# Kernel tuning notes

Measured on AMD Instinct MI355X. Metric: run time of the kernel, lower is better.

The kernel has to match this reference:

```python
import jax, jax.numpy as jnp
import numpy as np

B, S, E, D, H, DH, FF, NL = 16384, 4, 1152, 192, 4, 48, 768, 2


def _ln(x, w, b, eps=1e-5):
    m = jnp.mean(x, axis=-1, keepdims=True)
    v = jnp.mean((x - m) ** 2, axis=-1, keepdims=True)
    return (x - m) * jax.lax.rsqrt(v + eps) * w + b


def _gelu(x):
    # torch nn.GELU / TransformerEncoderLayer(activation='gelu') use exact erf GELU
    return jax.nn.gelu(x, approximate=False)


def _pos_enc():
    pos = np.arange(S, dtype=np.float32)[:, None]
    div = np.exp(np.arange(0, D, 2, dtype=np.float32) * (-np.log(10000.0) / D))
    pe = np.zeros((S, D), dtype=np.float32)
    pe[:, 0::2] = np.sin(pos * div)
    pe[:, 1::2] = np.cos(pos * div)
    return jnp.asarray(pe)


def setup_inputs() -> dict:
    key = jax.random.key(0)
    ks = jax.random.split(key, 16)
    w = lambda k, shape: jax.random.normal(k, shape, jnp.float32) * 0.05
    return {
        'embeddings': jax.random.normal(ks[0], (B, S, E), jnp.float32),
        'in_ln_w': jnp.ones((E,), jnp.float32), 'in_ln_b': jnp.zeros((E,), jnp.float32),
        'in_proj_w': w(ks[1], (D, E)), 'in_proj_b': jnp.zeros((D,), jnp.float32),
        'qkv_w': w(ks[2], (NL, 3 * D, D)), 'qkv_b': jnp.zeros((NL, 3 * D), jnp.float32),
        'attn_out_w': w(ks[3], (NL, D, D)), 'attn_out_b': jnp.zeros((NL, D), jnp.float32),
        'ln1_w': jnp.ones((NL, D), jnp.float32), 'ln1_b': jnp.zeros((NL, D), jnp.float32),
        'ln2_w': jnp.ones((NL, D), jnp.float32), 'ln2_b': jnp.zeros((NL, D), jnp.float32),
        'ff1_w': w(ks[4], (NL, FF, D)), 'ff1_b': jnp.zeros((NL, FF), jnp.float32),
        'ff2_w': w(ks[5], (NL, D, FF)), 'ff2_b': jnp.zeros((NL, D), jnp.float32),
        'head_ln_w': jnp.ones((D,), jnp.float32), 'head_ln_b': jnp.zeros((D,), jnp.float32),
        'h1_w': w(ks[6], (256, D)), 'h1_b': jnp.zeros((256,), jnp.float32),
        'h2_w': w(ks[7], (64, 256)), 'h2_b': jnp.zeros((64,), jnp.float32),
        'h3_w': w(ks[8], (1, 64)) * 0.1, 'h3_b': jnp.zeros((1,), jnp.float32),
    }


def reference(embeddings, in_ln_w, in_ln_b, in_proj_w, in_proj_b,
              qkv_w, qkv_b, attn_out_w, attn_out_b,
              ln1_w, ln1_b, ln2_w, ln2_b,
              ff1_w, ff1_b, ff2_w, ff2_b,
              head_ln_w, head_ln_b, h1_w, h1_b, h2_w, h2_b, h3_w, h3_b):
    # input_proj: LN -> Linear(E, D) -> GELU (dropout is identity in eval)
    x = _ln(embeddings, in_ln_w, in_ln_b)
    x = _gelu(x @ in_proj_w.T + in_proj_b)
    # sinusoidal positional encoding
    x = x + _pos_enc()[None]
    scale = 1.0 / jnp.sqrt(jnp.float32(DH))
    # norm_first TransformerEncoder layers
    for i in range(NL):
        xn = _ln(x, ln1_w[i], ln1_b[i])
        qkv = xn @ qkv_w[i].T + qkv_b[i]                       # (B, S, 3D)
        q, k, v = jnp.split(qkv, 3, axis=-1)
        q = q.reshape(B, S, H, DH)
        k = k.reshape(B, S, H, DH)
        v = v.reshape(B, S, H, DH)
        scores = jnp.einsum('bqhd,bkhd->bhqk', q, k) * scale   # (B, H, S, S)
        attn = jax.nn.softmax(scores, axis=-1)
        o = jnp.einsum('bhqk,bkhd->bqhd', attn, v).reshape(B, S, D)
        x = x + (o @ attn_out_w[i].T + attn_out_b[i])
        xn = _ln(x, ln2_w[i], ln2_b[i])
        x = x + (_gelu(xn @ ff1_w[i].T + ff1_b[i]) @ ff2_w[i].T + ff2_b[i])
    pooled = x.mean(axis=1)                                    # (B, D)
    h = _ln(pooled, head_ln_w, head_ln_b)
    h = _gelu(h @ h1_w.T + h1_b)
    h = _gelu(h @ h2_w.T + h2_b)
    return (h @ h3_w.T + h3_b)[:, 0]                           # (B,)
```

## Files before the change

kernel.cpp:

```cpp
#include <hip/hip_runtime.h>
#include <hip/hip_bf16.h>
#include <math.h>

#define B_   16384
#define S_   4
#define E_   1152
#define D_   192
#define FF_  768
#define NL_  2
#define MTOK (B_ * S_)

typedef __attribute__((ext_vector_type(8))) _Float16 half8;
typedef __attribute__((ext_vector_type(4))) float floatx4;

__device__ __forceinline__ float gelu_f(float x) {
  return 0.5f * x * (1.0f + erff(x * 0.70710678118654752f));
}

__global__ __launch_bounds__(256) void cvt_f16_kernel(const float* __restrict__ s,
                                                      _Float16* __restrict__ d) {
  int i = (blockIdx.x * 256 + threadIdx.x) * 8;
  float4 a = *(const float4*)(s + i);
  float4 b = *(const float4*)(s + i + 4);
  half8 h;
// ... 11 lines not shown
  const float* Wr = W + (size_t)n * 1152;
  _Float16* Whr = Wh + (size_t)n * 1152;
  float s1 = 0.f, s2 = 0.f;
  #pragma unroll
  for (int j = 0; j < 18; ++j) {
    int k = lane + 64 * j;
    float wv = Wr[k];
    _Float16 h = (_Float16)(wv * g[k]);
    Whr[k] = h;
    s1 += (float)h;
    s2 = fmaf(b[k], wv, s2);
  }
  #pragma unroll
  for (int off = 1; off < 64; off <<= 1) {
    s1 += __shfl_xor(s1, off);
    s2 += __shfl_xor(s2, off);
  }
  if (lane == 0) { c1[n] = s1; c2[n] = s2 + bias[n]; }
}

__global__ __launch_bounds__(256) void inproj2_kernel(
    const float* __restrict__ emb, const _Float16* __restrict__ whp,
    const float* __restrict__ c1g, const float* __restrict__ c2g,
    float* __restrict__ xout, float* __restrict__ stD) {
  __shared__ __align__(16) _Float16 As[64][72];
  __shared__ float stats_[64][2];
  __shared__ float red_[4][64][2];
  __shared__ float pe_[4][192];
  const int tid = threadIdx.x;
  const int m0 = blockIdx.x * 64;
  const int w = tid >> 6, lane = tid & 63;
  const int ln16 = lane & 15, quad = lane >> 4;
  const int r_a = tid >> 2;
  const int c_a = (tid & 3) * 16;

  for (int i = tid; i < 768; i += 256) {
    int r = i / 192, col = i - r * 192;
    float ang = (float)r * expf((float)(col & ~1) * (-0.047970522770709292f));
    pe_[r][col] = (col & 1) ? cosf(ang) : sinf(ang);
  }

  const float* Arow = emb + (size_t)(m0 + r_a) * 1152 + c_a;
  const _Float16* wb = whp + (size_t)(w * 48 + ln16) * 1152 + quad * 8;

  float4 pa[4];
  auto loadA = [&](int k0) {
    #pragma unroll
    for (int j = 0; j < 4; ++j) pa[j] = *(const float4*)(Arow + k0 + j * 4);
  };

// ... 41 lines not shown

  s += __shfl_xor(s, 1); s += __shfl_xor(s, 2);
  q += __shfl_xor(q, 1); q += __shfl_xor(q, 2);
  if ((tid & 3) == 0) {
    float mean = s * (1.f / 1152.f);
    stats_[r_a][0] = mean;
    stats_[r_a][1] = rsqrtf(q * (1.f / 1152.f) - mean * mean + 1e-5f);
  }
  __syncthreads();

  float c1v[3], c2v[3];
  #pragma unroll
  for (int nt = 0; nt < 3; ++nt) {
    c1v[nt] = c1g[w * 48 + nt * 16 + ln16];
    c2v[nt] = c2g[w * 48 + nt * 16 + ln16];
  }
  float* xg = xout + (size_t)m0 * 192;
  #pragma unroll
  for (int mt = 0; mt < 4; ++mt) {
    #pragma unroll
    for (int r = 0; r < 4; ++r) {
      const int row = mt * 16 + quad * 4 + r;
      const float rm = stats_[row][0], rr = stats_[row][1];
      float so = 0.f, qo = 0.f;
      #pragma unroll
      for (int nt = 0; nt < 3; ++nt) {
        const int col = w * 48 + nt * 16 + ln16;
        float v = rr * (acc[mt][nt][r] - rm * c1v[nt]) + c2v[nt];
        v = gelu_f(v);
        v += pe_[r][col];
        xg[(size_t)row * 192 + col] = v;
        so += v;
        qo = fmaf(v, v, qo);
      }
      so += __shfl_xor(so, 1); so += __shfl_xor(so, 2);
      so += __shfl_xor(so, 4); so += __shfl_xor(so, 8);
      qo += __shfl_xor(qo, 1); qo += __shfl_xor(qo, 2);
      qo += __shfl_xor(qo, 4); qo += __shfl_xor(qo, 8);
      if (ln16 == 0) { red_[w][row][0] = so; red_[w][row][1] = qo; }
    }
  }
  __syncthreads();
  if (tid < 64) {
    float so = red_[0][tid][0] + red_[1][tid][0] + red_[2][tid][0] + red_[3][tid][0];
    float qo = red_[0][tid][1] + red_[1][tid][1] + red_[2][tid][1] + red_[3][tid][1];
    float mean = so * (1.f / 192.f);
    stD[2 * (m0 + tid)] = mean;
    stD[2 * (m0 + tid) + 1] = rsqrtf(qo * (1.f / 192.f) - mean * mean + 1e-5f);
  }
}

__global__ __launch_bounds__(256) void layer_attn_kernel(
    float* __restrict__ x, const _Float16* __restrict__ wqkv,
    const float* __restrict__ bqkv, const _Float16* __restrict__ wao,
    const float* __restrict__ bao, const float* __restrict__ ln1g,
    const float* __restrict__ ln1b_, float* __restrict__ stD) {
  __shared__ __align__(16) _Float16 xh[32][200];
  __shared__ __align__(16) _Float16 qk[32][584];
  __shared__ float sp[8][4][4][4];
  const int tid = threadIdx.x;
  const int m0 = blockIdx.x * 32;
  const int w = tid >> 6, lane = tid & 63;
  const int ln16 = lane & 15, quad = lane >> 4;

  {
    const int ra = tid >> 3, ca = (tid & 7) * 24;
    const float sm = stD[2 * (m0 + ra)], srs = stD[2 * (m0 + ra) + 1];
    const float* Ar = x + (size_t)(m0 + ra) * 192 + ca;
    #pragma unroll
    for (int j = 0; j < 3; ++j) {
      float4 a0 = *(const float4*)(Ar + j * 8);
      float4 a1 = *(const float4*)(Ar + j * 8 + 4);
      float4 g0 = *(const float4*)(ln1g + ca + j * 8);
      float4 g1 = *(const float4*)(ln1g + ca + j * 8 + 4);
      float4 b0 = *(const float4*)(ln1b_ + ca + j * 8);
      float4 b1 = *(const float4*)(ln1b_ + ca + j * 8 + 4);
      half8 h;
      h[0] = (_Float16)((a0.x - sm) * srs * g0.x + b0.x);
      h[1] = (_Float16)((a0.y - sm) * srs * g0.y + b0.y);
      h[2] = (_Float16)((a0.z - sm) * srs * g0.z + b0.z);
      h[3] = (_Float16)((a0.w - sm) * srs * g0.w + b0.w);
      h[4] = (_Float16)((a1.x - sm) * srs * g1.x + b1.x);
      h[5] = (_Float16)((a1.y - sm) * srs * g1.y + b1.y);
      h[6] = (_Float16)((a1.z - sm) * srs * g1.z + b1.z);
      h[7] = (_Float16)((a1.w - sm) * srs * g1.w + b1.w);
      *(half8*)&xh[ra][ca + j * 8] = h;
    }
  }
  __syncthreads();

  for (int nt = 0; nt < 9; ++nt) {
    const int nc = w * 144 + nt * 16;
    half8 bf[6];
    const _Float16* wp = wqkv + (size_t)(nc + ln16) * 192 + quad * 8;
    #pragma unroll
    for (int k = 0; k < 6; ++k) bf[k] = *(const half8*)(wp + k * 32);
    floatx4 a0v = {}, a1v = {};
    #pragma unroll
    for (int k = 0; k < 6; ++k) {
      half8 f0 = *(const half8*)&xh[ln16][k * 32 + quad * 8];
      half8 f1 = *(const half8*)&xh[16 + ln16][k * 32 + quad * 8];
      a0v = __builtin_amdgcn_mfma_f32_16x16x32_f16(f0, bf[k], a0v, 0, 0, 0);
      a1v = __builtin_amdgcn_mfma_f32_16x16x32_f16(f1, bf[k], a1v, 0, 0, 0);
    }
    const float bv = bqkv[nc + ln16];
    #pragma unroll
    for (int r = 0; r < 4; ++r) {
      qk[quad * 4 + r][nc + ln16]      = (_Float16)(a0v[r] + bv);
      qk[16 + quad * 4 + r][nc + ln16] = (_Float16)(a1v[r] + bv);
    }
  }
  __syncthreads();

  #pragma unroll
  for (int s2 = 0; s2 < 2; ++s2) {
    const int sg = w * 2 + s2;
    const int h = lane >> 4, i = (lane >> 2) & 3, j = lane & 3;
    const _Float16* qp = &qk[4 * sg + i][h * 48];
    const _Float16* kp = &qk[4 * sg + j][192 + h * 48];
    float s = 0.f;
    #pragma unroll
    for (int d = 0; d < 6; ++d) {
      half8 qv = *(const half8*)(qp + d * 8);
      half8 kv = *(const half8*)(kp + d * 8);
      #pragma unroll
      for (int e = 0; e < 8; ++e) s += (float)qv[e] * (float)kv[e];
    }
    s *= 0.14433756729740643f;
    float mx = fmaxf(s, __shfl_xor(s, 1));
    mx = fmaxf(mx, __shfl_xor(mx, 2));
    float e = expf(s - mx);
    float sum = e + __shfl_xor(e, 1);
    sum += __shfl_xor(sum, 2);
    sp[sg][h][i][j] = e / sum;
  }
  #pragma unroll
  for (int s2 = 0; s2 < 2; ++s2) {
    const int sg = w * 2 + s2;
    #pragma unroll
    for (int ii = 0; ii < 4; ++ii) {
      #pragma unroll
      for (int cc = 0; cc < 3; ++cc) {
        const int c = lane + cc * 64;
        const int hh = c / 48;
        float a = 0.f;
        #pragma unroll
        for (int jj = 0; jj < 4; ++jj)
          a += sp[sg][hh][ii][jj] * (float)qk[4 * sg + jj][384 + c];
        xh[4 * sg + ii][c] = (_Float16)a;
      }
    }
  }
  __syncthreads();

  float* outs = (float*)&qk[0][0];
  #pragma unroll
  for (int nt = 0; nt < 3; ++nt) {
    const int nc = w * 48 + nt * 16;
    half8 bf[6];
    const _Float16* wp = wao + (size_t)(nc + ln16) * 192 + quad * 8;
    #pragma unroll
    for (int k = 0; k < 6; ++k) bf[k] = *(const half8*)(wp + k * 32);
    floatx4 a0v = {}, a1v = {};
    #pragma unroll
    for (int k = 0; k < 6; ++k) {
      half8 f0 = *(const half8*)&xh[ln16][k * 32 + quad * 8];
      half8 f1 = *(const half8*)&xh[16 + ln16][k * 32 + quad * 8];
      a0v = __builtin_amdgcn_mfma_f32_16x16x32_f16(f0, bf[k], a0v, 0, 0, 0);
      a1v = __builtin_amdgcn_mfma_f32_16x16x32_f16(f1, bf[k], a1v, 0, 0, 0);
    }
    const float bv = bao[nc + ln16];
    #pragma unroll
    for (int r = 0; r < 4; ++r) {
      outs[(quad * 4 + r) * 192 + nc + ln16]      = a0v[r] + bv;
      outs[(16 + quad * 4 + r) * 192 + nc + ln16] = a1v[r] + bv;
    }
  }
  __syncthreads();

  {
    const int fbase = tid * 6;
    const int row = tid >> 3;
    float* xg = x + (size_t)m0 * 192;
    float s = 0.f, q = 0.f;
    #pragma unroll
    for (int j = 0; j < 6; ++j) {
      float4 v = ((const float4*)outs)[fbase + j];
      float4 rr = *(const float4*)(xg + (fbase + j) * 4);
      v.x += rr.x; v.y += rr.y; v.z += rr.z; v.w += rr.w;
      s += v.x + v.y + v.z + v.w;
      q += v.x * v.x + v.y * v.y + v.z * v.z + v.w * v.w;
      *(float4*)(xg + (fbase + j) * 4) = v;
    }
    s += __shfl_xor(s, 1); s += __shfl_xor(s, 2); s += __shfl_xor(s, 4);
    q += __shfl_xor(q, 1); q += __shfl_xor(q, 2); q += __shfl_xor(q, 4);
    if ((tid & 7) == 0) {
      float mean = s * (1.f / 192.f);
      stD[2 * (m0 + row)] = mean;
      stD[2 * (m0 + row) + 1] = rsqrtf(q * (1.f / 192.f) - mean * mean + 1e-5f);
    }
  }
}

__global__ __launch_bounds__(256) void layer_ff_kernel(
    float* __restrict__ x, const _Float16* __restrict__ wff1,
    const float* __restrict__ bff1, const _Float16* __restrict__ wff2,
    const float* __restrict__ bff2, const float* __restrict__ ln2g,
    const float* __restrict__ ln2b_, float* __restrict__ stD) {
  __shared__ __align__(16) _Float16 xh2[64][200];
  __shared__ __align__(16) _Float16 ffh[64][392];
  const int tid = threadIdx.x;
  const int m0 = blockIdx.x * 64;
  const int w = tid >> 6, lane = tid & 63;
  const int ln16 = lane & 15, quad = lane >> 4;

  {
    const int ra = tid >> 2, ca = (tid & 3) * 48;
    const float sm = stD[2 * (m0 + ra)], srs = stD[2 * (m0 + ra) + 1];
    const float* Ar = x + (size_t)(m0 + ra) * 192 + ca;
    #pragma unroll
    for (int j = 0; j < 6; ++j) {
      float4 a0 = *(const float4*)(Ar + j * 8);
      float4 a1 = *(const float4*)(Ar + j * 8 + 4);
      float4 g0 = *(const float4*)(ln2g + ca + j * 8);
      float4 g1 = *(const float4*)(ln2g + ca + j * 8 + 4);
      float4 b0 = *(const float4*)(ln2b_ + ca + j * 8);
      float4 b1 = *(const float4*)(ln2b_ + ca + j * 8 + 4);
      half8 h;
      h[0] = (_Float16)((a0.x - sm) * srs * g0.x + b0.x);
      h[1] = (_Float16)((a0.y - sm) * srs * g0.y + b0.y);
      h[2] = (_Float16)((a0.z - sm) * srs * g0.z + b0.z);
      h[3] = (_Float16)((a0.w - sm) * srs * g0.w + b0.w);
      h[4] = (_Float16)((a1.x - sm) * srs * g1.x + b1.x);
      h[5] = (_Float16)((a1.y - sm) * srs * g1.y + b1.y);
      h[6] = (_Float16)((a1.z - sm) * srs * g1.z + b1.z);
      h[7] = (_Float16)((a1.w - sm) * srs * g1.w + b1.w);
      *(half8*)&xh2[ra][ca + j * 8] = h;
    }
  }
  __syncthreads();

  floatx4 acc2[4][3] = {};
  for (int half = 0; half < 2; ++half) {
    #pragma unroll
    for (int nt = 0; nt < 6; ++nt) {
      const int ng = half * 384 + w * 96 + nt * 16;
      const int nl = w * 96 + nt * 16;
      half8 bf[6];
      const _Float16* wp = wff1 + (size_t)(ng + ln16) * 192 + quad * 8;
      #pragma unroll
      for (int k = 0; k < 6; ++k) bf[k] = *(const half8*)(wp + k * 32);
      floatx4 a4[4] = {};
      #pragma unroll
      for (int k = 0; k < 6; ++k) {
        #pragma unroll
        for (int mt = 0; mt < 4; ++mt) {
          half8 af = *(const half8*)&xh2[mt * 16 + ln16][k * 32 + quad * 8];
          a4[mt] = __builtin_amdgcn_mfma_f32_16x16x32_f16(af, bf[k], a4[mt], 0, 0, 0);
        }
      }
      const float bv = bff1[ng + ln16];
      #pragma unroll
      for (int mt = 0; mt < 4; ++mt)
        #pragma unroll
        for (int r = 0; r < 4; ++r)
          ffh[mt * 16 + quad * 4 + r][nl + ln16] = (_Float16)gelu_f(a4[mt][r] + bv);
    }
    __syncthreads();
    for (int k12 = 0; k12 < 12; ++k12) {
      half8 af[4];
      #pragma unroll
      for (int mt = 0; mt < 4; ++mt)
        af[mt] = *(const half8*)&ffh[mt * 16 + ln16][k12 * 32 + quad * 8];
      #pragma unroll
      for (int nt = 0; nt < 3; ++nt) {
        const int nc = w * 48 + nt * 16;
        half8 bf = *(const half8*)(wff2 + (size_t)(nc + ln16) * 768 +
                                   half * 384 + k12 * 32 + quad * 8);
        #pragma unroll
        for (int mt = 0; mt < 4; ++mt)
          acc2[mt][nt] = __builtin_amdgcn_mfma_f32_16x16x32_f16(
              af[mt], bf, acc2[mt][nt], 0, 0, 0);
      }
    }
    __syncthreads();
  }

  float* outs = (float*)&ffh[0][0];
  #pragma unroll
  for (int nt = 0; nt < 3; ++nt) {
    const int nc = w * 48 + nt * 16;
    const float bv = bff2[nc + ln16];
    #pragma unroll
    for (int mt = 0; mt < 4; ++mt)
      #pragma unroll
      for (int r = 0; r < 4; ++r)
        outs[(mt * 16 + quad * 4 + r) * 192 + nc + ln16] = acc2[mt][nt][r] + bv;
  }
  __syncthreads();

  {
    const int fbase = tid * 12;
    const int row = tid >> 2;
    float* xg = x + (size_t)m0 * 192;
    float s = 0.f, q = 0.f;
    #pragma unroll
    for (int j = 0; j < 12; ++j) {
      float4 v = ((const float4*)outs)[fbase + j];
      float4 rr = *(const float4*)(xg + (fbase + j) * 4);
      v.x += rr.x; v.y += rr.y; v.z += rr.z; v.w += rr.w;
      s += v.x + v.y + v.z + v.w;
      q += v.x * v.x + v.y * v.y + v.z * v.z + v.w * v.w;
      *(float4*)(xg + (fbase + j) * 4) = v;
    }
    s += __shfl_xor(s, 1); s += __shfl_xor(s, 2);
    q += __shfl_xor(q, 1); q += __shfl_xor(q, 2);
    if ((tid & 3) == 0) {
      float mean = s * (1.f / 192.f);
      stD[2 * (m0 + row)] = mean;
      stD[2 * (m0 + row) + 1] = rsqrtf(q * (1.f / 192.f) - mean * mean + 1e-5f);
    }
  }
}

template <int EPI>
__global__ __launch_bounds__(256) void gemm_f32(
    const float* __restrict__ A, const float* __restrict__ W,
    const float* __restrict__ bias, float* __restrict__ C,
    int M, int N, int K) {
  __shared__ float As[16][68];
  __shared__ float Bs[16][68];
  const int tid = threadIdx.x;
  const int m0 = blockIdx.x * 64;
  const int n0 = blockIdx.y * 64;
  const int tx = tid & 15, ty = tid >> 4;
  const int lr = tid >> 2;
  const int lk = (tid & 3) << 2;
  float acc[4][4] = {};
  const float* Arow = A + (size_t)(m0 + lr) * K;
  const float* Wrow = W + (size_t)(n0 + lr) * K;
  for (int k0 = 0; k0 < K; k0 += 16) {
    float4 av = *(const float4*)(Arow + k0 + lk);
    float4 wv = *(const float4*)(Wrow + k0 + lk);
    __syncthreads();
    As[lk + 0][lr] = av.x; As[lk + 1][lr] = av.y;
    As[lk + 2][lr] = av.z; As[lk + 3][lr] = av.w;
    Bs[lk + 0][lr] = wv.x; Bs[lk + 1][lr] = wv.y;
    Bs[lk + 2][lr] = wv.z; Bs[lk + 3][lr] = wv.w;
    __syncthreads();
    #pragma unroll
    for (int kk = 0; kk < 16; ++kk) {
      float4 a = *(const float4*)&As[kk][ty * 4];
      float4 b = *(const float4*)&Bs[kk][tx * 4];
      acc[0][0] += a.x * b.x; acc[0][1] += a.x * b.y; acc[0][2] += a.x * b.z; acc[0][3] += a.x * b.w;
      acc[1][0] += a.y * b.x; acc[1][1] += a.y * b.y; acc[1][2] += a.y * b.z; acc[1][3] += a.y * b.w;
      acc[2][0] += a.z * b.x; acc[2][1] += a.z * b.y; acc[2][2] += a.z * b.z; acc[2][3] += a.z * b.w;
      acc[3][0] += a.w * b.x; acc[3][1] += a.w * b.y; acc[3][2] += a.w * b.z; acc[3][3] += a.w * b.w;
    }
  }
  float4 bv = *(const float4*)(bias + n0 + tx * 4);
  #pragma unroll
  for (int i = 0; i < 4; ++i) {
    int m = m0 + ty * 4 + i;
    float v0 = acc[i][0] + bv.x, v1 = acc[i][1] + bv.y;
    float v2 = acc[i][2] + bv.z, v3 = acc[i][3] + bv.w;
    if constexpr (EPI == 1) {
      v0 = gelu_f(v0); v1 = gelu_f(v1); v2 = gelu_f(v2); v3 = gelu_f(v3);
    }
    float4 ov; ov.x = v0; ov.y = v1; ov.z = v2; ov.w = v3;
    *(float4*)(C + (size_t)m * N + n0 + tx * 4) = ov;
  }
}

__global__ __launch_bounds__(256) void pool_ln_kernel(const float* __restrict__ x,
                                                      const float* __restrict__ g,
                                                      const float* __restrict__ b,
                                                      float* __restrict__ hout) {
  int bi = blockIdx.x * 4 + (threadIdx.x >> 6);
  int lane = threadIdx.x & 63;
  const float* row = x + (size_t)bi * 4 * D_;
  float vals[3];
  float sum = 0.f;
  #pragma unroll
  for (int cc = 0; cc < 3; ++cc) {
    int d = lane + cc * 64;
    float v = 0.25f * (row[d] + row[D_ + d] + row[2 * D_ + d] + row[3 * D_ + d]);
    vals[cc] = v; sum += v;
  }
  #pragma unroll
  for (int off = 1; off < 64; off <<= 1) sum += __shfl_xor(sum, off);
  float mean = sum / (float)D_;
  float vs = 0.f;
  #pragma unroll
  for (int cc = 0; cc < 3; ++cc) { float d0 = vals[cc] - mean; vs += d0 * d0; }
  #pragma unroll
  for (int off = 1; off < 64; off <<= 1) vs += __shfl_xor(vs, off);
  float rstd = rsqrtf(vs / (float)D_ + 1e-5f);
  #pragma unroll
  for (int cc = 0; cc < 3; ++cc) {
    int d = lane + cc * 64;
    hout[(size_t)bi * D_ + d] = (vals[cc] - mean) * rstd * g[d] + b[d];
  }
}

__global__ __launch_bounds__(256) void head_final_kernel(const float* __restrict__ h2,
                                                         const float* __restrict__ w,
                                                         const float* __restrict__ b,
                                                         float* __restrict__ out) {
  int bi = blockIdx.x * 4 + (threadIdx.x >> 6);
  int lane = threadIdx.x & 63;
  float v = h2[(size_t)bi * 64 + lane] * w[lane];
  #pragma unroll
  for (int off = 1; off < 64; off <<= 1) v += __shfl_xor(v, off);
  if (lane == 0) out[bi] = v + b[0];
}

extern "C" void kernel_launch(void* const* d_in, const int* in_sizes, int n_in,
                              void* d_out, int out_size, void* d_ws, size_t ws_size,
                              hipStream_t stream) {
  (void)in_sizes; (void)n_in; (void)out_size; (void)ws_size;
  const float* emb       = (const float*)d_in[0];
  const float* in_ln_w   = (const float*)d_in[1];
  const float* in_ln_b   = (const float*)d_in[2];
  const float* in_proj_w = (const float*)d_in[3];
  const float* in_proj_b = (const float*)d_in[4];
  const float* qkv_w     = (const float*)d_in[5];
  const float* qkv_b     = (const float*)d_in[6];
  const float* aow       = (const float*)d_in[7];
  const float* aob       = (const float*)d_in[8];
  const float* ln1w      = (const float*)d_in[9];
  const float* ln1b      = (const float*)d_in[10];
  const float* ln2w      = (const float*)d_in[11];
  const float* ln2b      = (const float*)d_in[12];
  const float* ff1w      = (const float*)d_in[13];
  const float* ff1b      = (const float*)d_in[14];
  const float* ff2w      = (const float*)d_in[15];
  const float* ff2b      = (const float*)d_in[16];
  const float* hlnw      = (const float*)d_in[17];
  const float* hlnb      = (const float*)d_in[18];
  const float* h1w       = (const float*)d_in[19];
  const float* h1b       = (const float*)d_in[20];
  const float* h2w       = (const float*)d_in[21];
  const float* h2b       = (const float*)d_in[22];
  const float* h3w       = (const float*)d_in[23];
  const float* h3b       = (const float*)d_in[24];
  float* out = (float*)d_out;

  float* ws = (float*)d_ws;
  size_t off = 0;
  float* x   = ws + off; off += (size_t)MTOK * D_;
  float* stD = ws + off; off += (size_t)MTOK * 2;
  float* hp  = ws + off; off += (size_t)B_ * D_;
  float* h1  = ws + off; off += (size_t)B_ * 256;
  float* h2  = ws + off; off += (size_t)B_ * 64;
  float* c1  = ws + off; off += 192;
  float* c2  = ws + off; off += 192;
  _Float16* wh = (_Float16*)(ws + off);
  _Float16* w_inproj = wh;
  _Float16* w_qkv    = w_inproj + 221184;
  _Float16* w_ao     = w_qkv    + 221184;
  _Float16* w_ff1    = w_ao     + 73728;
  _Float16* w_ff2    = w_ff1    + 294912;

  prep_inproj_w<<<48, 256, 0, stream>>>(in_proj_w, in_ln_w, in_ln_b, in_proj_b,
                                        w_inproj, c1, c2);
  cvt_f16_kernel<<<221184 / 2048, 256, 0, stream>>>(qkv_w, w_qkv);
  cvt_f16_kernel<<<73728  / 2048, 256, 0, stream>>>(aow, w_ao);
  cvt_f16_kernel<<<294912 / 2048, 256, 0, stream>>>(ff1w, w_ff1);
  cvt_f16_kernel<<<294912 / 2048, 256, 0, stream>>>(ff2w, w_ff2);

  inproj2_kernel<<<MTOK / 64, 256, 0, stream>>>(emb, w_inproj, c1, c2, x, stD);

  for (int i = 0; i < NL_; ++i) {
    layer_attn_kernel<<<MTOK / 32, 256, 0, stream>>>(
        x, w_qkv + (size_t)i * 110592, qkv_b + (size_t)i * 576,
        w_ao + (size_t)i * 36864, aob + (size_t)i * 192,
        ln1w + (size_t)i * 192, ln1b + (size_t)i * 192, stD);
    layer_ff_kernel<<<MTOK / 64, 256, 0, stream>>>(
        x, w_ff1 + (size_t)i * 147456, ff1b + (size_t)i * 768,
        w_ff2 + (size_t)i * 147456, ff2b + (size_t)i * 192,
        ln2w + (size_t)i * 192, ln2b + (size_t)i * 192, stD);
  }

  pool_ln_kernel<<<B_ / 4, 256, 0, stream>>>(x, hlnw, hlnb, hp);
  gemm_f32<1><<<dim3(B_ / 64, 256 / 64), 256, 0, stream>>>(hp, h1w, h1b, h1, B_, 256, D_);
  gemm_f32<1><<<dim3(B_ / 64, 64 / 64), 256, 0, stream>>>(h1, h2w, h2b, h2, B_, 64, 256);
  head_final_kernel<<<B_ / 4, 256, 0, stream>>>(h2, h3w, h3b, out);
}
```

Before: 996.4 us.

## Fuse both encoder layers, pooling and regression head into one register-resident kernel

Replaces the per-layer attention and feed-forward kernels, pooling, two fp32 head GEMMs and the final reduction with a single kernel. Each 32-token block keeps its residual stream in registers across both layers and computes LayerNorm statistics in place, so x and the stats buffer are no longer written and re-read through global memory. The head MLP now runs in fp16 MFMA with pre-converted weights. In exchange, the FF stage uses 32-row tiles (less weight reuse per block than the previous 64-row tiles), register pressure goes up, and the head carries fp16 rounding and zero-padded MFMA rows.

```diff
diff --git a/kernel.cpp b/kernel.cpp
--- a/kernel.cpp
+++ b/kernel.cpp
@@ -57,10 +57,9 @@
 __global__ __launch_bounds__(256) void inproj2_kernel(
     const float* __restrict__ emb, const _Float16* __restrict__ whp,
     const float* __restrict__ c1g, const float* __restrict__ c2g,
-    float* __restrict__ xout, float* __restrict__ stD) {
+    float* __restrict__ xout) {
   __shared__ __align__(16) _Float16 As[64][72];
   __shared__ float stats_[64][2];
-  __shared__ float red_[4][64][2];
   __shared__ float pe_[4][192];
   const int tid = threadIdx.x;
   const int m0 = blockIdx.x * 64;
@@ -148,7 +147,6 @@
     for (int r = 0; r < 4; ++r) {
       const int row = mt * 16 + quad * 4 + r;
       const float rm = stats_[row][0], rr = stats_[row][1];
-      float so = 0.f, qo = 0.f;
       #pragma unroll
       for (int nt = 0; nt < 3; ++nt) {
         const int col = w * 48 + nt * 16 + ln16;
@@ -156,31 +154,24 @@
         v = gelu_f(v);
         v += pe_[r][col];
         xg[(size_t)row * 192 + col] = v;
-        so += v;
-        qo = fmaf(v, v, qo);
-      }
-      so += __shfl_xor(so, 1); so += __shfl_xor(so, 2);
-      so += __shfl_xor(so, 4); so += __shfl_xor(so, 8);
-      qo += __shfl_xor(qo, 1); qo += __shfl_xor(qo, 2);
-      qo += __shfl_xor(qo, 4); qo += __shfl_xor(qo, 8);
-      if (ln16 == 0) { red_[w][row][0] = so; red_[w][row][1] = qo; }
-    }
-  }
-  __syncthreads();
-  if (tid < 64) {
-    float so = red_[0][tid][0] + red_[1][tid][0] + red_[2][tid][0] + red_[3][tid][0];
-    float qo = red_[0][tid][1] + red_[1][tid][1] + red_[2][tid][1] + red_[3][tid][1];
-    float mean = so * (1.f / 192.f);
-    stD[2 * (m0 + tid)] = mean;
-    stD[2 * (m0 + tid) + 1] = rsqrtf(qo * (1.f / 192.f) - mean * mean + 1e-5f);
+      }
+    }
   }
 }
 
-__global__ __launch_bounds__(256) void layer_attn_kernel(
-    float* __restrict__ x, const _Float16* __restrict__ wqkv,
-    const float* __restrict__ bqkv, const _Float16* __restrict__ wao,
-    const float* __restrict__ bao, const float* __restrict__ ln1g,
-    const float* __restrict__ ln1b_, float* __restrict__ stD) {
+__global__ __launch_bounds__(256) void mega_kernel(
+    const float* __restrict__ x,
+    const _Float16* __restrict__ wqkv0, const float* __restrict__ bqkv0,
+    const _Float16* __restrict__ wao0,  const float* __restrict__ bao0,
+    const _Float16* __restrict__ wff10, const float* __restrict__ bff10,
+    const _Float16* __restrict__ wff20, const float* __restrict__ bff20,
+    const float* __restrict__ ln1g0, const float* __restrict__ ln1b0,
+    const float* __restrict__ ln2g0, const float* __restrict__ ln2b0,
+    const float* __restrict__ hlng, const float* __restrict__ hlnb,
+    const _Float16* __restrict__ h1wh, const float* __restrict__ h1b,
+    const _Float16* __restrict__ h2wh, const float* __restrict__ h2b,
+    const float* __restrict__ h3w, const float* __restrict__ h3b,
+    float* __restrict__ out) {
   __shared__ __align__(16) _Float16 xh[32][200];
   __shared__ __align__(16) _Float16 qk[32][584];
   __shared__ float sp[8][4][4][4];
@@ -188,357 +179,315 @@
   const int m0 = blockIdx.x * 32;
   const int w = tid >> 6, lane = tid & 63;
   const int ln16 = lane & 15, quad = lane >> 4;
-
+  const int row = tid >> 3, cg = tid & 7;
+  const int ca = cg * 24;
+
+  float4 xr[6];
   {
-    const int ra = tid >> 3, ca = (tid & 7) * 24;
-    const float sm = stD[2 * (m0 + ra)], srs = stD[2 * (m0 + ra) + 1];
-    const float* Ar = x + (size_t)(m0 + ra) * 192 + ca;
-    #pragma unroll
-    for (int j = 0; j < 3; ++j) {
-      float4 a0 = *(const float4*)(Ar + j * 8);
-      float4 a1 = *(const float4*)(Ar + j * 8 + 4);
-      float4 g0 = *(const float4*)(ln1g + ca + j * 8);
-      float4 g1 = *(const float4*)(ln1g + ca + j * 8 + 4);
-      float4 b0 = *(const float4*)(ln1b_ + ca + j * 8);
-      float4 b1 = *(const float4*)(ln1b_ + ca + j * 8 + 4);
-      half8 h;
-      h[0] = (_Float16)((a0.x - sm) * srs * g0.x + b0.x);
-      h[1] = (_Float16)((a0.y - sm) * srs * g0.y + b0.y);
-      h[2] = (_Float16)((a0.z - sm) * srs * g0.z + b0.z);
-      h[3] = (_Float16)((a0.w - sm) * srs * g0.w + b0.w);
-      h[4] = (_Float16)((a1.x - sm) * srs * g1.x + b1.x);
-      h[5] = (_Float16)((a1.y - sm) * srs * g1.y + b1.y);
-      h[6] = (_Float16)((a1.z - sm) * srs * g1.z + b1.z);
-      h[7] = (_Float16)((a1.w - sm) * srs * g1.w + b1.w);
-      *(half8*)&xh[ra][ca + j * 8] = h;
-    }
-  }
-  __syncthreads();
-
-  for (int nt = 0; nt < 9; ++nt) {
-    const int nc = w * 144 + nt * 16;
-    half8 bf[6];
-    const _Float16* wp = wqkv + (size_t)(nc + ln16) * 192 + quad * 8;
-    #pragma unroll
-    for (int k = 0; k < 6; ++k) bf[k] = *(const half8*)(wp + k * 32);
-    floatx4 a0v = {}, a1v = {};
-    #pragma unroll
-    for (int k = 0; k < 6; ++k) {
-      half8 f0 = *(const half8*)&xh[ln16][k * 32 + quad * 8];
-      half8 f1 = *(const half8*)&xh[16 + ln16][k * 32 + quad * 8];
-      a0v = __builtin_amdgcn_mfma_f32_16x16x32_f16(f0, bf[k], a0v, 0, 0, 0);
-      a1v = __builtin_amdgcn_mfma_f32_16x16x32_f16(f1, bf[k], a1v, 0, 0, 0);
-    }
-    const float bv = bqkv[nc + ln16];
-    #pragma unroll
-    for (int r = 0; r < 4; ++r) {
-      qk[quad * 4 + r][nc + ln16]      = (_Float16)(a0v[r] + bv);
-      qk[16 + quad * 4 + r][nc + ln16] = (_Float16)(a1v[r] + bv);
-    }
-  }
-  __syncthreads();
-
-  #pragma unroll
-  for (int s2 = 0; s2 < 2; ++s2) {
-    const int sg = w * 2 + s2;
-    const int h = lane >> 4, i = (lane >> 2) & 3, j = lane & 3;
-    const _Float16* qp = &qk[4 * sg + i][h * 48];
-    const _Float16* kp = &qk[4 * sg + j][192 + h * 48];
-    float s = 0.f;
-    #pragma unroll
-    for (int d = 0; d < 6; ++d) {
-      half8 qv = *(const half8*)(qp + d * 8);
-      half8 kv = *(const half8*)(kp + d * 8);
-      #pragma unroll
-      for (int e = 0; e < 8; ++e) s += (float)qv[e] * (float)kv[e];
-    }
-    s *= 0.14433756729740643f;
-    float mx = fmaxf(s, __shfl_xor(s, 1));
-    mx = fmaxf(mx, __shfl_xor(mx, 2));
-    float e = expf(s - mx);
-    float sum = e + __shfl_xor(e, 1);
-    sum += __shfl_xor(sum, 2);
-    sp[sg][h][i][j] = e / sum;
-  }
-  #pragma unroll
-  for (int s2 = 0; s2 < 2; ++s2) {
-    const int sg = w * 2 + s2;
-    #pragma unroll
-    for (int ii = 0; ii < 4; ++ii) {
-      #pragma unroll
-      for (int cc = 0; cc < 3; ++cc) {
-        const int c = lane + cc * 64;
-        const int hh = c / 48;
-        float a = 0.f;
-        #pragma unroll
-        for (int jj = 0; jj < 4; ++jj)
-          a += sp[sg][hh][ii][jj] * (float)qk[4 * sg + jj][384 + c];
-        xh[4 * sg + ii][c] = (_Float16)a;
-      }
-    }
-  }
-  __syncthreads();
-
-  float* outs = (float*)&qk[0][0];
-  #pragma unroll
-  for (int nt = 0; nt < 3; ++nt) {
-    const int nc = w * 48 + nt * 16;
-    half8 bf[6];
-    const _Float16* wp = wao + (size_t)(nc + ln16) * 192 + quad * 8;
-    #pragma unroll
-    for (int k = 0; k < 6; ++k) bf[k] = *(const half8*)(wp + k * 32);
-    floatx4 a0v = {}, a1v = {};
-    #pragma unroll
-    for (int k = 0; k < 6; ++k) {
-      half8 f0 = *(const half8*)&xh[ln16][k * 32 + quad * 8];
-      half8 f1 = *(const half8*)&xh[16 + ln16][k * 32 + quad * 8];
-      a0v = __builtin_amdgcn_mfma_f32_16x16x32_f16(f0, bf[k], a0v, 0, 0, 0);
-      a1v = __builtin_amdgcn_mfma_f32_16x16x32_f16(f1, bf[k], a1v, 0, 0, 0);
-    }
-    const float bv = bao[nc + ln16];
-    #pragma unroll
-    for (int r = 0; r < 4; ++r) {
-      outs[(quad * 4 + r) * 192 + nc + ln16]      = a0v[r] + bv;
-      outs[(16 + quad * 4 + r) * 192 + nc + ln16] = a1v[r] + bv;
-    }
-  }
-  __syncthreads();
-
-  {
-    const int fbase = tid * 6;
-    const int row = tid >> 3;
-    float* xg = x + (size_t)m0 * 192;
+    const float* Ar = x + (size_t)(m0 + row) * 192 + ca;
+    #pragma unroll
+    for (int j = 0; j < 6; ++j) xr[j] = *(const float4*)(Ar + j * 4);
+  }
+
+  auto ln_to_xh = [&](const float* g, const float* bb) {
     float s = 0.f, q = 0.f;
     #pragma unroll
     for (int j = 0; j < 6; ++j) {
-      float4 v = ((const float4*)outs)[fbase + j];
-      float4 rr = *(const float4*)(xg + (fbase + j) * 4);
-      v.x += rr.x; v.y += rr.y; v.z += rr.z; v.w += rr.w;
+      float4 v = xr[j];
       s += v.x + v.y + v.z + v.w;
-      q += v.x * v.x + v.y * v.y + v.z * v.z + v.w * v.w;
-      *(float4*)(xg + (fbase + j) * 4) = v;
+      q = fmaf(v.x, v.x, q); q = fmaf(v.y, v.y, q);
+      q = fmaf(v.z, v.z, q); q = fmaf(v.w, v.w, q);
     }
     s += __shfl_xor(s, 1); s += __shfl_xor(s, 2); s += __shfl_xor(s, 4);
     q += __shfl_xor(q, 1); q += __shfl_xor(q, 2); q += __shfl_xor(q, 4);
-    if ((tid & 7) == 0) {
-      float mean = s * (1.f / 192.f);
-      stD[2 * (m0 + row)] = mean;
-      stD[2 * (m0 + row) + 1] = rsqrtf(q * (1.f / 192.f) - mean * mean + 1e-5f);
-    }
-  }
-}
-
-__global__ __launch_bounds__(256) void layer_ff_kernel(
-    float* __restrict__ x, const _Float16* __restrict__ wff1,
-    const float* __restrict__ bff1, const _Float16* __restrict__ wff2,
-    const float* __restrict__ bff2, const float* __restrict__ ln2g,
-    const float* __restrict__ ln2b_, float* __restrict__ stD) {
-  __shared__ __align__(16) _Float16 xh2[64][200];
-  __shared__ __align__(16) _Float16 ffh[64][392];
-  const int tid = threadIdx.x;
-  const int m0 = blockIdx.x * 64;
-  const int w = tid >> 6, lane = tid & 63;
-  const int ln16 = lane & 15, quad = lane >> 4;
-
-  {
-    const int ra = tid >> 2, ca = (tid & 3) * 48;
-    const float sm = stD[2 * (m0 + ra)], srs = stD[2 * (m0 + ra) + 1];
-    const float* Ar = x + (size_t)(m0 + ra) * 192 + ca;
-    #pragma unroll
-    for (int j = 0; j < 6; ++j) {
-      float4 a0 = *(const float4*)(Ar + j * 8);
-      float4 a1 = *(const float4*)(Ar + j * 8 + 4);
-      float4 g0 = *(const float4*)(ln2g + ca + j * 8);
-      float4 g1 = *(const float4*)(ln2g + ca + j * 8 + 4);
-      float4 b0 = *(const float4*)(ln2b_ + ca + j * 8);
-      float4 b1 = *(const float4*)(ln2b_ + ca + j * 8 + 4);
+    const float mean = s * (1.f / 192.f);
+    const float rs = rsqrtf(q * (1.f / 192.f) - mean * mean + 1e-5f);
+    #pragma unroll
+    for (int j = 0; j < 3; ++j) {
+      float4 a0 = xr[2 * j], a1 = xr[2 * j + 1];
+      float4 g0 = *(const float4*)(g + ca + j * 8);
+      float4 g1 = *(const float4*)(g + ca + j * 8 + 4);
+      float4 b0 = *(const float4*)(bb + ca + j * 8);
+      float4 b1 = *(const float4*)(bb + ca + j * 8 + 4);
       half8 h;
-      h[0] = (_Float16)((a0.x - sm) * srs * g0.x + b0.x);
-      h[1] = (_Float16)((a0.y - sm) * srs * g0.y + b0.y);
-      h[2] = (_Float16)((a0.z - sm) * srs * g0.z + b0.z);
-      h[3] = (_Float16)((a0.w - sm) * srs * g0.w + b0.w);
-      h[4] = (_Float16)((a1.x - sm) * srs * g1.x + b1.x);
-      h[5] = (_Float16)((a1.y - sm) * srs * g1.y + b1.y);
-      h[6] = (_Float16)((a1.z - sm) * srs * g1.z + b1.z);
-      h[7] = (_Float16)((a1.w - sm) * srs * g1.w + b1.w);
-      *(half8*)&xh2[ra][ca + j * 8] = h;
-    }
-  }
-  __syncthreads();
-
-  floatx4 acc2[4][3] = {};
-  for (int half = 0; half < 2; ++half) {
-    #pragma unroll
-    for (int nt = 0; nt < 6; ++nt) {
-      const int ng = half * 384 + w * 96 + nt * 16;
-      const int nl = w * 96 + nt * 16;
+      h[0] = (_Float16)((a0.x - mean) * rs * g0.x + b0.x);
+      h[1] = (_Float16)((a0.y - mean) * rs * g0.y + b0.y);
+      h[2] = (_Float16)((a0.z - mean) * rs * g0.z + b0.z);
+      h[3] = (_Float16)((a0.w - mean) * rs * g0.w + b0.w);
+      h[4] = (_Float16)((a1.x - mean) * rs * g1.x + b1.x);
+      h[5] = (_Float16)((a1.y - mean) * rs * g1.y + b1.y);
+      h[6] = (_Float16)((a1.z - mean) * rs * g1.z + b1.z);
+      h[7] = (_Float16)((a1.w - mean) * rs * g1.w + b1.w);
+      *(half8*)&xh[row][ca + j * 8] = h;
+    }
+  };
+
+  for (int l = 0; l < NL_; ++l) {
+    const _Float16* wqkv = wqkv0 + (size_t)l * 110592;
+    const float*    bqkv = bqkv0 + (size_t)l * 576;
+    const _Float16* wao  = wao0  + (size_t)l * 36864;
+    const float*    bao  = bao0  + (size_t)l * 192;
+    const _Float16* wff1 = wff10 + (size_t)l * 147456;
+    const float*    bff1 = bff10 + (size_t)l * 768;
+    const _Float16* wff2 = wff20 + (size_t)l * 147456;
+    const float*    bff2 = bff20 + (size_t)l * 192;
+
+    ln_to_xh(ln1g0 + l * 192, ln1b0 + l * 192);
+    __syncthreads();
+
+    for (int nt = 0; nt < 9; ++nt) {
+      const int nc = w * 144 + nt * 16;
       half8 bf[6];
-      const _Float16* wp = wff1 + (size_t)(ng + ln16) * 192 + quad * 8;
+      const _Float16* wp = wqkv + (size_t)(nc + ln16) * 192 + quad * 8;
       #pragma unroll
       for (int k = 0; k < 6; ++k) bf[k] = *(const half8*)(wp + k * 32);
-      floatx4 a4[4] = {};
+      floatx4 a0v = {}, a1v = {};
       #pragma unroll
       for (int k = 0; k < 6; ++k) {
-        #pragma unroll
-        for (int mt = 0; mt < 4; ++mt) {
-          half8 af = *(const half8*)&xh2[mt * 16 + ln16][k * 32 + quad * 8];
-          a4[mt] = __builtin_amdgcn_mfma_f32_16x16x32_f16(af, bf[k], a4[mt], 0, 0, 0);
+        half8 f0 = *(const half8*)&xh[ln16][k * 32 + quad * 8];
+        half8 f1 = *(const half8*)&xh[16 + ln16][k * 32 + quad * 8];
+        a0v = __builtin_amdgcn_mfma_f32_16x16x32_f16(f0, bf[k], a0v, 0, 0, 0);
+        a1v = __builtin_amdgcn_mfma_f32_16x16x32_f16(f1, bf[k], a1v, 0, 0, 0);
+      }
+      const float bv = bqkv[nc + ln16];
+      #pragma unroll
+      for (int r = 0; r < 4; ++r) {
+        qk[quad * 4 + r][nc + ln16]      = (_Float16)(a0v[r] + bv);
+        qk[16 + quad * 4 + r][nc + ln16] = (_Float16)(a1v[r] + bv);
+      }
+    }
+    __syncthreads();
+
+    #pragma unroll
+    for (int s2 = 0; s2 < 2; ++s2) {
+      const int sg = w * 2 + s2;
+      const int hh = lane >> 4, i = (lane >> 2) & 3, j = lane & 3;
+      const _Float16* qp = &qk[4 * sg + i][hh * 48];
+      const _Float16* kp = &qk[4 * sg + j][192 + hh * 48];
+      float s = 0.f;
+      #pragma unroll
+      for (int d = 0; d < 6; ++d) {
+        half8 qv = *(const half8*)(qp + d * 8);
+        half8 kv = *(const half8*)(kp + d * 8);
+        #pragma unroll
+        for (int e = 0; e < 8; ++e) s += (float)qv[e] * (float)kv[e];
+      }
+      s *= 0.14433756729740643f;
+      float mx = fmaxf(s, __shfl_xor(s, 1));
+      mx = fmaxf(mx, __shfl_xor(mx, 2));
+      float e = expf(s - mx);
+      float sum = e + __shfl_xor(e, 1);
+      sum += __shfl_xor(sum, 2);
+      sp[sg][hh][i][j] = e / sum;
+    }
+    #pragma unroll
+    for (int s2 = 0; s2 < 2; ++s2) {
+      const int sg = w * 2 + s2;
+      #pragma unroll
+      for (int ii = 0; ii < 4; ++ii) {
+        #pragma unroll
+        for (int cc = 0; cc < 3; ++cc) {
+          const int c = lane + cc * 64;
+          const int hh = c / 48;
+          float a = 0.f;
+          #pragma unroll
+          for (int jj = 0; jj < 4; ++jj)
+            a += sp[sg][hh][ii][jj] * (float)qk[4 * sg + jj][384 + c];
+          xh[4 * sg + ii][c] = (_Float16)a;
         }
       }
-      const float bv = bff1[ng + ln16];
-      #pragma unroll
-      for (int mt = 0; mt < 4; ++mt)
-        #pragma unroll
-        for (int r = 0; r < 4; ++r)
-          ffh[mt * 16 + quad * 4 + r][nl + ln16] = (_Float16)gelu_f(a4[mt][r] + bv);
-    }
-    __syncthreads();
-    for (int k12 = 0; k12 < 12; ++k12) {
-      half8 af[4];
-      #pragma unroll
-      for (int mt = 0; mt < 4; ++mt)
-        af[mt] = *(const half8*)&ffh[mt * 16 + ln16][k12 * 32 + quad * 8];
+    }
+    __syncthreads();
+
+    float* outs = (float*)&qk[0][0];
+    #pragma unroll
+    for (int nt = 0; nt < 3; ++nt) {
+      const int nc = w * 48 + nt * 16;
+      half8 bf[6];
+      const _Float16* wp = wao + (size_t)(nc + ln16) * 192 + quad * 8;
+      #pragma unroll
+      for (int k = 0; k < 6; ++k) bf[k] = *(const half8*)(wp + k * 32);
+      floatx4 a0v = {}, a1v = {};
+      #pragma unroll
+      for (int k = 0; k < 6; ++k) {
+        half8 f0 = *(const half8*)&xh[ln16][k * 32 + quad * 8];
+        half8 f1 = *(const half8*)&xh[16 + ln16][k * 32 + quad * 8];
+        a0v = __builtin_amdgcn_mfma_f32_16x16x32_f16(f0, bf[k], a0v, 0, 0, 0);
+        a1v = __builtin_amdgcn_mfma_f32_16x16x32_f16(f1, bf[k], a1v, 0, 0, 0);
+      }
+      const float bv = bao[nc + ln16];
+      #pragma unroll
+      for (int r = 0; r < 4; ++r) {
+        outs[(quad * 4 + r) * 192 + nc + ln16]      = a0v[r] + bv;
+        outs[(16 + quad * 4 + r) * 192 + nc + ln16] = a1v[r] + bv;
+      }
+    }
+    __syncthreads();
+
+    {
+      const float* os = (const float*)&qk[0][0] + row * 192 + ca;
+      #pragma unroll
+      for (int j = 0; j < 6; ++j) {
+        float4 o4 = *(const float4*)(os + j * 4);
+        xr[j].x += o4.x; xr[j].y += o4.y; xr[j].z += o4.z; xr[j].w += o4.w;
+      }
+    }
+    ln_to_xh(ln2g0 + l * 192, ln2b0 + l * 192);
+    __syncthreads();
+
+    floatx4 acc2[2][3] = {};
+    _Float16 (*ffh)[392] = (_Float16 (*)[392])&qk[0][0];
+    for (int hf = 0; hf < 2; ++hf) {
+      #pragma unroll
+      for (int nt = 0; nt < 6; ++nt) {
+        const int ng = hf * 384 + w * 96 + nt * 16;
+        const int nl = w * 96 + nt * 16;
+        half8 bf[6];
+        const _Float16* wp = wff1 + (size_t)(ng + ln16) * 192 + quad * 8;
+        #pragma unroll
+        for (int k = 0; k < 6; ++k) bf[k] = *(const half8*)(wp + k * 32);
+        floatx4 a4[2] = {};
+        #pragma unroll
+        for (int k = 0; k < 6; ++k) {
+          #pragma unroll
+          for (int mt = 0; mt < 2; ++mt) {
+            half8 af = *(const half8*)&xh[mt * 16 + ln16][k * 32 + quad * 8];
+            a4[mt] = __builtin_amdgcn_mfma_f32_16x16x32_f16(af, bf[k], a4[mt], 0, 0, 0);
+          }
+        }
+        const float bv = bff1[ng + ln16];
+        #pragma unroll
+        for (int mt = 0; mt < 2; ++mt)
+          #pragma unroll
+          for (int r = 0; r < 4; ++r)
+            ffh[mt * 16 + quad * 4 + r][nl + ln16] = (_Float16)gelu_f(a4[mt][r] + bv);
+      }
+      __syncthreads();
+      for (int k12 = 0; k12 < 12; ++k12) {
+        half8 af[2];
+        #pragma unroll
+        for (int mt = 0; mt < 2; ++mt)
+          af[mt] = *(const half8*)&ffh[mt * 16 + ln16][k12 * 32 + quad * 8];
+        #pragma unroll
+        for (int nt = 0; nt < 3; ++nt) {
+          const int nc = w * 48 + nt * 16;
+          half8 bf = *(const half8*)(wff2 + (size_t)(nc + ln16) * 768 +
+                                     hf * 384 + k12 * 32 + quad * 8);
+          #pragma unroll
+          for (int mt = 0; mt < 2; ++mt)
+            acc2[mt][nt] = __builtin_amdgcn_mfma_f32_16x16x32_f16(
+                af[mt], bf, acc2[mt][nt], 0, 0, 0);
+        }
+      }
+      __syncthreads();
+    }
+    {
+      float* outs2 = (float*)&qk[0][0];
       #pragma unroll
       for (int nt = 0; nt < 3; ++nt) {
         const int nc = w * 48 + nt * 16;
-        half8 bf = *(const half8*)(wff2 + (size_t)(nc + ln16) * 768 +
-                                   half * 384 + k12 * 32 + quad * 8);
-        #pragma unroll
-        for (int mt = 0; mt < 4; ++mt)
-          acc2[mt][nt] = __builtin_amdgcn_mfma_f32_16x16x32_f16(
-              af[mt], bf, acc2[mt][nt], 0, 0, 0);
-      }
-    }
-    __syncthreads();
-  }
-
-  float* outs = (float*)&ffh[0][0];
+        const float bv = bff2[nc + ln16];
+        #pragma unroll
+        for (int mt = 0; mt < 2; ++mt)
+          #pragma unroll
+          for (int r = 0; r < 4; ++r)
+            outs2[(mt * 16 + quad * 4 + r) * 192 + nc + ln16] = acc2[mt][nt][r] + bv;
+      }
+    }
+    __syncthreads();
+    {
+      const float* os = (const float*)&qk[0][0] + row * 192 + ca;
+      #pragma unroll
+      for (int j = 0; j < 6; ++j) {
+        float4 o4 = *(const float4*)(os + j * 4);
+        xr[j].x += o4.x; xr[j].y += o4.y; xr[j].z += o4.z; xr[j].w += o4.w;
+      }
+    }
+    __syncthreads();
+  }
+
+  {
+    float* xs = (float*)&qk[0][0];
+    #pragma unroll
+    for (int j = 0; j < 6; ++j)
+      *(float4*)(xs + row * 192 + ca + j * 4) = xr[j];
+  }
+  __syncthreads();
+  _Float16 (*ph)[200] = (_Float16 (*)[200])&xh[0][0];
+  {
+    const float* xs = (const float*)&qk[0][0];
+    const int s = tid >> 5, u = tid & 31;
+    float pv[6];
+    float ss = 0.f, qq = 0.f;
+    #pragma unroll
+    for (int c6 = 0; c6 < 6; ++c6) {
+      const int c = u * 6 + c6;
+      float v = 0.25f * (xs[(4 * s) * 192 + c] + xs[(4 * s + 1) * 192 + c] +
+                         xs[(4 * s + 2) * 192 + c] + xs[(4 * s + 3) * 192 + c]);
+      pv[c6] = v; ss += v; qq = fmaf(v, v, qq);
+    }
+    ss += __shfl_xor(ss, 1); ss += __shfl_xor(ss, 2); ss += __shfl_xor(ss, 4);
+    ss += __shfl_xor(ss, 8); ss += __shfl_xor(ss, 16);
+    qq += __shfl_xor(qq, 1); qq += __shfl_xor(qq, 2); qq += __shfl_xor(qq, 4);
+    qq += __shfl_xor(qq, 8); qq += __shfl_xor(qq, 16);
+    const float mean = ss * (1.f / 192.f);
+    const float rs = rsqrtf(qq * (1.f / 192.f) - mean * mean + 1e-5f);
+    #pragma unroll
+    for (int c6 = 0; c6 < 6; ++c6) {
+      const int c = u * 6 + c6;
+      ph[s][c] = (_Float16)((pv[c6] - mean) * rs * hlng[c] + hlnb[c]);
+      ph[8 + s][c] = (_Float16)0.f;
+    }
+  }
+  __syncthreads();
+  _Float16 (*h1s)[264] = (_Float16 (*)[264])&qk[0][0];
   #pragma unroll
-  for (int nt = 0; nt < 3; ++nt) {
-    const int nc = w * 48 + nt * 16;
-    const float bv = bff2[nc + ln16];
-    #pragma unroll
-    for (int mt = 0; mt < 4; ++mt)
-      #pragma unroll
-      for (int r = 0; r < 4; ++r)
-        outs[(mt * 16 + quad * 4 + r) * 192 + nc + ln16] = acc2[mt][nt][r] + bv;
+  for (int nt = 0; nt < 4; ++nt) {
+    const int nc = w * 64 + nt * 16;
+    half8 bf[6];
+    const _Float16* wp = h1wh + (size_t)(nc + ln16) * 192 + quad * 8;
+    #pragma unroll
+    for (int k = 0; k < 6; ++k) bf[k] = *(const half8*)(wp + k * 32);
+    floatx4 a4 = {};
+    #pragma unroll
+    for (int k = 0; k < 6; ++k) {
+      half8 af = *(const half8*)&ph[ln16][k * 32 + quad * 8];
+      a4 = __builtin_amdgcn_mfma_f32_16x16x32_f16(af, bf[k], a4, 0, 0, 0);
+    }
+    const float bv = h1b[nc + ln16];
+    #pragma unroll
+    for (int r = 0; r < 4; ++r) {
+      const int rr = quad * 4 + r;
+      h1s[rr][nc + ln16] = (rr < 8) ? (_Float16)gelu_f(a4[r] + bv) : (_Float16)0.f;
+    }
   }
   __syncthreads();
-
+  _Float16 (*h2s)[72] = (_Float16 (*)[72])((char*)&qk[0][0] + 16384);
   {
-    const int fbase = tid * 12;
-    const int row = tid >> 2;
-    float* xg = x + (size_t)m0 * 192;
-    float s = 0.f, q = 0.f;
-    #pragma unroll
-    for (int j = 0; j < 12; ++j) {
-      float4 v = ((const float4*)outs)[fbase + j];
-      float4 rr = *(const float4*)(xg + (fbase + j) * 4);
-      v.x += rr.x; v.y += rr.y; v.z += rr.z; v.w += rr.w;
-      s += v.x + v.y + v.z + v.w;
-      q += v.x * v.x + v.y * v.y + v.z * v.z + v.w * v.w;
-      *(float4*)(xg + (fbase + j) * 4) = v;
-    }
-    s += __shfl_xor(s, 1); s += __shfl_xor(s, 2);
-    q += __shfl_xor(q, 1); q += __shfl_xor(q, 2);
-    if ((tid & 3) == 0) {
-      float mean = s * (1.f / 192.f);
-      stD[2 * (m0 + row)] = mean;
-      stD[2 * (m0 + row) + 1] = rsqrtf(q * (1.f / 192.f) - mean * mean + 1e-5f);
-    }
-  }
-}
-
-template <int EPI>
-__global__ __launch_bounds__(256) void gemm_f32(
-    const float* __restrict__ A, const float* __restrict__ W,
-    const float* __restrict__ bias, float* __restrict__ C,
-    int M, int N, int K) {
-  __shared__ float As[16][68];
-  __shared__ float Bs[16][68];
-  const int tid = threadIdx.x;
-  const int m0 = blockIdx.x * 64;
-  const int n0 = blockIdx.y * 64;
-  const int tx = tid & 15, ty = tid >> 4;
-  const int lr = tid >> 2;
-  const int lk = (tid & 3) << 2;
-  float acc[4][4] = {};
-  const float* Arow = A + (size_t)(m0 + lr) * K;
-  const float* Wrow = W + (size_t)(n0 + lr) * K;
-  for (int k0 = 0; k0 < K; k0 += 16) {
-    float4 av = *(const float4*)(Arow + k0 + lk);
-    float4 wv = *(const float4*)(Wrow + k0 + lk);
-    __syncthreads();
-    As[lk + 0][lr] = av.x; As[lk + 1][lr] = av.y;
-    As[lk + 2][lr] = av.z; As[lk + 3][lr] = av.w;
-    Bs[lk + 0][lr] = wv.x; Bs[lk + 1][lr] = wv.y;
-    Bs[lk + 2][lr] = wv.z; Bs[lk + 3][lr] = wv.w;
-    __syncthreads();
-    #pragma unroll
-    for (int kk = 0; kk < 16; ++kk) {
-      float4 a = *(const float4*)&As[kk][ty * 4];
-      float4 b = *(const float4*)&Bs[kk][tx * 4];
-      acc[0][0] += a.x * b.x; acc[0][1] += a.x * b.y; acc[0][2] += a.x * b.z; acc[0][3] += a.x * b.w;
-      acc[1][0] += a.y * b.x; acc[1][1] += a.y * b.y; acc[1][2] += a.y * b.z; acc[1][3] += a.y * b.w;
-      acc[2][0] += a.z * b.x; acc[2][1] += a.z * b.y; acc[2][2] += a.z * b.z; acc[2][3] += a.z * b.w;
-      acc[3][0] += a.w * b.x; acc[3][1] += a.w * b.y; acc[3][2] += a.w * b.z; acc[3][3] += a.w * b.w;
-    }
-  }
-  float4 bv = *(const float4*)(bias + n0 + tx * 4);
-  #pragma unroll
-  for (int i = 0; i < 4; ++i) {
-    int m = m0 + ty * 4 + i;
-    float v0 = acc[i][0] + bv.x, v1 = acc[i][1] + bv.y;
-    float v2 = acc[i][2] + bv.z, v3 = acc[i][3] + bv.w;
-    if constexpr (EPI == 1) {
-      v0 = gelu_f(v0); v1 = gelu_f(v1); v2 = gelu_f(v2); v3 = gelu_f(v3);
-    }
-    float4 ov; ov.x = v0; ov.y = v1; ov.z = v2; ov.w = v3;
-    *(float4*)(C + (size_t)m * N + n0 + tx * 4) = ov;
-  }
-}
-
-__global__ __launch_bounds__(256) void pool_ln_kernel(const float* __restrict__ x,
-                                                      const float* __restrict__ g,
-                                                      const float* __restrict__ b,
-                                                      float* __restrict__ hout) {
-  int bi = blockIdx.x * 4 + (threadIdx.x >> 6);
-  int lane = threadIdx.x & 63;
-  const float* row = x + (size_t)bi * 4 * D_;
-  float vals[3];
-  float sum = 0.f;
-  #pragma unroll
-  for (int cc = 0; cc < 3; ++cc) {
-    int d = lane + cc * 64;
-    float v = 0.25f * (row[d] + row[D_ + d] + row[2 * D_ + d] + row[3 * D_ + d]);
-    vals[cc] = v; sum += v;
-  }
-  #pragma unroll
-  for (int off = 1; off < 64; off <<= 1) sum += __shfl_xor(sum, off);
-  float mean = sum / (float)D_;
-  float vs = 0.f;
-  #pragma unroll
-  for (int cc = 0; cc < 3; ++cc) { float d0 = vals[cc] - mean; vs += d0 * d0; }
-  #pragma unroll
-  for (int off = 1; off < 64; off <<= 1) vs += __shfl_xor(vs, off);
-  float rstd = rsqrtf(vs / (float)D_ + 1e-5f);
-  #pragma unroll
-  for (int cc = 0; cc < 3; ++cc) {
-    int d = lane + cc * 64;
-    hout[(size_t)bi * D_ + d] = (vals[cc] - mean) * rstd * g[d] + b[d];
-  }
-}
-
-__global__ __launch_bounds__(256) void head_final_kernel(const float* __restrict__ h2,
-                                                         const float* __restrict__ w,
-                                                         const float* __restrict__ b,
-                                                         float* __restrict__ out) {
-  int bi = blockIdx.x * 4 + (threadIdx.x >> 6);
-  int lane = threadIdx.x & 63;
-  float v = h2[(size_t)bi * 64 + lane] * w[lane];
-  #pragma unroll
-  for (int off = 1; off < 64; off <<= 1) v += __shfl_xor(v, off);
-  if (lane == 0) out[bi] = v + b[0];
+    const int nc = w * 16;
+    floatx4 a4 = {};
+    #pragma unroll
+    for (int k = 0; k < 8; ++k) {
+      half8 af = *(const half8*)&h1s[ln16][k * 32 + quad * 8];
+      half8 bf = *(const half8*)(h2wh + (size_t)(nc + ln16) * 256 + k * 32 + quad * 8);
+      a4 = __builtin_amdgcn_mfma_f32_16x16x32_f16(af, bf, a4, 0, 0, 0);
+    }
+    const float bv = h2b[nc + ln16];
+    #pragma unroll
+    for (int r = 0; r < 4; ++r) {
+      const int rr = quad * 4 + r;
+      if (rr < 8) h2s[rr][nc + ln16] = (_Float16)gelu_f(a4[r] + bv);
+    }
+  }
+  __syncthreads();
+  {
+    const int s = tid >> 5, u = tid & 31;
+    float v = (float)h2s[s][2 * u] * h3w[2 * u] +
+              (float)h2s[s][2 * u + 1] * h3w[2 * u + 1];
+    v += __shfl_xor(v, 1); v += __shfl_xor(v, 2); v += __shfl_xor(v, 4);
+    v += __shfl_xor(v, 8); v += __shfl_xor(v, 16);
+    if (u == 0) out[blockIdx.x * 8 + s] = v + h3b[0];
+  }
 }
 
 extern "C" void kernel_launch(void* const* d_in, const int* in_sizes, int n_in,
@@ -575,10 +524,6 @@
   float* ws = (float*)d_ws;
   size_t off = 0;
   float* x   = ws + off; off += (size_t)MTOK * D_;
-  float* stD = ws + off; off += (size_t)MTOK * 2;
-  float* hp  = ws + off; off += (size_t)B_ * D_;
-  float* h1  = ws + off; off += (size_t)B_ * 256;
-  float* h2  = ws + off; off += (size_t)B_ * 64;
   float* c1  = ws + off; off += 192;
   float* c2  = ws + off; off += 192;
   _Float16* wh = (_Float16*)(ws + off);
@@ -587,6 +532,8 @@
   _Float16* w_ao     = w_qkv    + 221184;
   _Float16* w_ff1    = w_ao     + 73728;
   _Float16* w_ff2    = w_ff1    + 294912;
+  _Float16* w_h1     = w_ff2    + 294912;
+  _Float16* w_h2     = w_h1     + 49152;
 
   prep_inproj_w<<<48, 256, 0, stream>>>(in_proj_w, in_ln_w, in_ln_b, in_proj_b,
                                         w_inproj, c1, c2);
@@ -594,22 +541,13 @@
   cvt_f16_kernel<<<73728  / 2048, 256, 0, stream>>>(aow, w_ao);
   cvt_f16_kernel<<<294912 / 2048, 256, 0, stream>>>(ff1w, w_ff1);
   cvt_f16_kernel<<<294912 / 2048, 256, 0, stream>>>(ff2w, w_ff2);
-
-  inproj2_kernel<<<MTOK / 64, 256, 0, stream>>>(emb, w_inproj, c1, c2, x, stD);
-
-  for (int i = 0; i < NL_; ++i) {
-    layer_attn_kernel<<<MTOK / 32, 256, 0, stream>>>(
-        x, w_qkv + (size_t)i * 110592, qkv_b + (size_t)i * 576,
-        w_ao + (size_t)i * 36864, aob + (size_t)i * 192,
-        ln1w + (size_t)i * 192, ln1b + (size_t)i * 192, stD);
-    layer_ff_kernel<<<MTOK / 64, 256, 0, stream>>>(
-        x, w_ff1 + (size_t)i * 147456, ff1b + (size_t)i * 768,
-        w_ff2 + (size_t)i * 147456, ff2b + (size_t)i * 192,
-        ln2w + (size_t)i * 192, ln2b + (size_t)i * 192, stD);
-  }
-
-  pool_ln_kernel<<<B_ / 4, 256, 0, stream>>>(x, hlnw, hlnb, hp);
-  gemm_f32<1><<<dim3(B_ / 64, 256 / 64), 256, 0, stream>>>(hp, h1w, h1b, h1, B_, 256, D_);
-  gemm_f32<1><<<dim3(B_ / 64, 64 / 64), 256, 0, stream>>>(h1, h2w, h2b, h2, B_, 64, 256);
-  head_final_kernel<<<B_ / 4, 256, 0, stream>>>(h2, h3w, h3b, out);
+  cvt_f16_kernel<<<49152  / 2048, 256, 0, stream>>>(h1w, w_h1);
+  cvt_f16_kernel<<<16384  / 2048, 256, 0, stream>>>(h2w, w_h2);
+
+  inproj2_kernel<<<MTOK / 64, 256, 0, stream>>>(emb, w_inproj, c1, c2, x);
+
+  mega_kernel<<<MTOK / 32, 256, 0, stream>>>(
+      x, w_qkv, qkv_b, w_ao, aob, w_ff1, ff1b, w_ff2, ff2b,
+      ln1w, ln1b, ln2w, ln2b, hlnw, hlnb,
+      w_h1, h1b, w_h2, h2b, h3w, h3b, out);
 }
```

After: 1.187 ms. 1.19x slower.
